# Kernel optimization log

Hardware: AMD Instinct MI355X
Metric: run time of the kernel (lower is better)

## Reference

```python
import jax, jax.numpy as jnp
import numpy as np

VEC = 64
HEADS = 16
DUP = 4
HIDDEN = VEC * HEADS * DUP  # 4096
EPS = 1e-12


def setup_inputs() -> dict:
    key = jax.random.key(0)
    ks = jax.random.split(key, 7)
    B, S, N = 4, 512, 512
    out_len = VEC * HEADS
    return {
        "embeddings": jax.random.normal(ks[0], (B, S, HIDDEN), jnp.float32),
        "keys": jax.random.normal(ks[1], (B, N, out_len), jnp.float32),
        "values": jax.random.normal(ks[2], (B, N, out_len), jnp.float32),
        "Wq": jax.random.normal(ks[3], (HIDDEN, HIDDEN), jnp.float32) * (1.0 / np.sqrt(HIDDEN)),
        "bq": jnp.zeros((HIDDEN,), jnp.float32),
        "Wre": jax.random.normal(ks[4], (HIDDEN, HIDDEN), jnp.float32) * (1.0 / np.sqrt(HIDDEN)),
        "bre": jnp.zeros((HIDDEN,), jnp.float32),
        "ln_g": jnp.ones((HIDDEN,), jnp.float32),
        "ln_b": jnp.zeros((HIDDEN,), jnp.float32),
    }


def reference(embeddings, keys, values, Wq, bq, Wre, bre, ln_g, ln_b):
    B, S, _ = embeddings.shape
    N = keys.shape[1]
    # query projection: (B,S,hidden) -> reshape to (B, S*DUP, VEC, HEADS) -> (B,H,S*DUP,VEC)
    q = embeddings @ Wq.T + bq
    q = q.reshape(B, S * DUP, VEC, HEADS).transpose(0, 3, 1, 2)
    # keys: (B,N,VEC*HEADS) -> (B,H,VEC,N); values -> (B,H,N,VEC)
    k = keys.reshape(B, N, VEC, HEADS).transpose(0, 3, 2, 1)
    v = values.reshape(B, N, VEC, HEADS).transpose(0, 3, 1, 2)
    scores = jnp.matmul(q, k) / np.sqrt(VEC).astype(np.float32)  # (B,H,S*DUP,N)
    probs = jax.nn.softmax(scores, axis=-1)
    out = jnp.matmul(probs, v)  # (B,H,S*DUP,VEC)
    # (B,H,S*DUP,VEC) -> (B,H,S,VEC*DUP) -> (B,S,H,VEC*DUP) -> (B,S,HIDDEN)
    out = out.reshape(B, HEADS, S, VEC * DUP).transpose(0, 2, 1, 3).reshape(B, S, HIDDEN)
    # LayerNorm (biased variance, torch semantics)
    mu = jnp.mean(out, axis=-1, keepdims=True)
    var = jnp.mean(jnp.square(out - mu), axis=-1, keepdims=True)
    ln = (out - mu) / jnp.sqrt(var + EPS) * ln_g + ln_b
    return ln @ Wre.T + bre
```

## Files before the change

### kernel.cpp

```cpp
#include <hip/hip_runtime.h>

typedef __attribute__((ext_vector_type(8))) _Float16 half8;
typedef __attribute__((ext_vector_type(4))) _Float16 half4;
typedef __attribute__((ext_vector_type(4))) float    floatx4;

#define GLD16(g, l)                                                            \
  __builtin_amdgcn_global_load_lds(                                            \
      (const __attribute__((address_space(1))) void*)(g),                      \
      (__attribute__((address_space(3))) void*)(l), 16, 0, 0)

__device__ __forceinline__ void cvt8(const float* __restrict__ in,
                                     _Float16* __restrict__ out, int i) {
  const float4* p = (const float4*)in + (size_t)i * 2;
  float4 a = p[0], b = p[1];
  half8 h;
  h[0] = (_Float16)a.x; h[1] = (_Float16)a.y; h[2] = (_Float16)a.z; h[3] = (_Float16)a.w;
  h[4] = (_Float16)b.x; h[5] = (_Float16)b.y; h[6] = (_Float16)b.z; h[7] = (_Float16)b.w;
  *(half8*)(out + (size_t)i * 8) = h;
}

__global__ __launch_bounds__(256) void prepA(const float* __restrict__ emb,
                                             const float* __restrict__ Wq,
                                             const float* __restrict__ keys,
                                             const float* __restrict__ values,
                                             _Float16* __restrict__ embH,
                                             _Float16* __restrict__ WqH,
                                             _Float16* __restrict__ Kh,
                                             _Float16* __restrict__ Vt) {
  const int bid = blockIdx.x, t = threadIdx.x;
  if (bid < 4096) {
    cvt8(emb, embH, bid * 256 + t);
  } else if (bid < 12288) {
    cvt8(Wq, WqH, (bid - 4096) * 256 + t);
  } else {
    const int tid = (bid - 12288) * 256 + t;
    {
      int v = tid & 63, n = (tid >> 6) & 511, h = (tid >> 15) & 15, b = tid >> 19;
      Kh[tid] = (_Float16)keys[((size_t)(b * 512 + n)) * 1024 + v * 16 + h];
    }
    {
      int n = tid & 511, v = (tid >> 9) & 63, h = (tid >> 15) & 15, b = tid >> 19;
      Vt[tid] = (_Float16)values[((size_t)(b * 512 + n)) * 1024 + v * 16 + h];
    }
  }
}

template <int MODE>
__global__ __launch_bounds__(256, 3) void gemm_bt(const _Float16* __restrict__ A,
                                                  const _Float16* __restrict__ Bw,
                                                  const float* __restrict__ bias,
                                                  float* __restrict__ Cf,
                                                  _Float16* __restrict__ H0,
                                                  _Float16* __restrict__ H1) {
  const int K = 4096;
  __shared__ _Float16 lA[128 * 64];
  __shared__ _Float16 lB[128 * 64];
  const int t = threadIdx.x, lane = t & 63, w = t >> 6;
  const int m0 = blockIdx.y * 128, n0 = blockIdx.x * 128;
  const int kb = blockIdx.z * 2048;
  const int wm = (w >> 1) * 64, wn = (w & 1) * 64;
  const int fr = lane & 15, fq = lane >> 4;

  floatx4 acc[4][4];
#pragma unroll
  for (int i = 0; i < 4; i++)
#pragma unroll
    for (int j = 0; j < 4; j++) acc[i][j] = (floatx4)(0.f);

  const int srow = t >> 3;
  const int sch = (t & 7) ^ (srow & 7);
  const _Float16* gA = A + (size_t)(m0 + srow) * K + kb + sch * 8;
  const _Float16* gB = Bw + (size_t)(n0 + srow) * K + kb + sch * 8;
  _Float16* dA = &lA[t * 8];
  _Float16* dB = &lB[t * 8];

  for (int k0 = 0; k0 < 2048; k0 += 64) {
    GLD16(gA, dA);
    GLD16(gA + (size_t)32 * K, dA + 2048);
    GLD16(gA + (size_t)64 * K, dA + 4096);
    GLD16(gA + (size_t)96 * K, dA + 6144);
    GLD16(gB, dB);
    GLD16(gB + (size_t)32 * K, dB + 2048);
    GLD16(gB + (size_t)64 * K, dB + 4096);
    GLD16(gB + (size_t)96 * K, dB + 6144);
    gA += 64;
    gB += 64;
    __syncthreads();
#pragma unroll
    for (int ks = 0; ks < 2; ks++) {
      half8 af[4], bf[4];
#pragma unroll
      for (int i = 0; i < 4; i++) {
        const int rr = wm + i * 16 + fr;
        af[i] = *(const half8*)&lA[rr * 64 + (((ks * 4 + fq) ^ (rr & 7)) * 8)];
      }
#pragma unroll
      for (int j = 0; j < 4; j++) {
        const int rr = wn + j * 16 + fr;
        bf[j] = *(const half8*)&lB[rr * 64 + (((ks * 4 + fq) ^ (rr & 7)) * 8)];
      }
#pragma unroll
      for (int i = 0; i < 4; i++)
#pragma unroll
        for (int j = 0; j < 4; j++)
          acc[i][j] =
              __builtin_amdgcn_mfma_f32_16x16x32_f16(af[i], bf[j], acc[i][j], 0, 0, 0);
    }
    __syncthreads();
  }

  const int z = blockIdx.z;
#pragma unroll
  for (int i = 0; i < 4; i++)
#pragma unroll
    for (int j = 0; j < 4; j++) {
      const int col = n0 + wn + j * 16 + fr;
      const int rbase = m0 + wm + i * 16 + fq * 4;
      if (MODE == 0 && z == 0) {
        const float bv = bias[col];
#pragma unroll
        for (int r = 0; r < 4; r++)
          Cf[(size_t)(rbase + r) * 4096 + col] = acc[i][j][r] + bv;
      } else {
        _Float16* P = z ? H1 : H0;
#pragma unroll
        for (int r = 0; r < 4; r++)
          P[(size_t)(rbase + r) * 4096 + col] = (_Float16)acc[i][j][r];
      }
    }
}

__global__ __launch_bounds__(256) void prepB(const float* __restrict__ Wre,
                                             _Float16* __restrict__ WreH,
                                             const _Float16* __restrict__ p0,
                                             const _Float16* __restrict__ p1,
                                             const float* __restrict__ bq,
                                             _Float16* __restrict__ q) {
  const int bid = blockIdx.x, t = threadIdx.x;
  if (bid < 8192) {
    cvt8(Wre, WreH, bid * 256 + t);
    return;
  }
  __shared__ _Float16 T[4][16][80];
  const int L = t & 63, w = t >> 6;
  const int m = bid - 8192, d = w;
  const int b = m >> 9, s = m & 511;
  const size_t src = (size_t)m * 4096 + d * 1024 + L * 16;
  half8 a0 = *(const half8*)(p0 + src);
  half8 a1 = *(const half8*)(p0 + src + 8);
  half8 b0 = *(const half8*)(p1 + src);
  half8 b1 = *(const half8*)(p1 + src + 8);
  const float4* bqv = (const float4*)(bq + d * 1024 + L * 16);
  float bias[16];
#pragma unroll
  for (int c = 0; c < 4; c++) {
    float4 f = bqv[c];
    bias[c * 4 + 0] = f.x; bias[c * 4 + 1] = f.y;
    bias[c * 4 + 2] = f.z; bias[c * 4 + 3] = f.w;
  }
#pragma unroll
  for (int h = 0; h < 8; h++) {
    T[w][h][L] = (_Float16)(((float)a0[h] + (float)b0[h] + bias[h]) * 0.125f);
    T[w][h + 8][L] =
        (_Float16)(((float)a1[h] + (float)b1[h] + bias[h + 8]) * 0.125f);
  }
  const int h2 = L >> 2, c2 = L & 3;
  _Float16* dst = q + (((size_t)(b * 16 + h2) * 2048) + s * 4 + d) * 64 + c2 * 8;
  *(half8*)dst = *(const half8*)&T[w][h2][c2 * 8];
  *(half8*)(dst + 32) = *(const half8*)&T[w][h2][32 + c2 * 8];
}

__global__ __launch_bounds__(256) void combine2(float* __restrict__ out,
                                                const _Float16* __restrict__ p1) {
  const int i4 = (blockIdx.x * 256 + threadIdx.x) * 4;
  float4 o = *(float4*)&out[i4];
  half4 p = *(const half4*)(p1 + i4);
  o.x += (float)p[0];
  o.y += (float)p[1];
  o.z += (float)p[2];
  o.w += (float)p[3];
  *(float4*)&out[i4] = o;
}

__global__ __launch_bounds__(256) void attn_mfma(const _Float16* __restrict__ Q,
                                                 const _Float16* __restrict__ Kh,
                                                 const _Float16* __restrict__ Vt,
                                                 float* __restrict__ Out) {
  __shared__ _Float16 Pbuf[4][32][136];
  const int t = threadIdx.x, lane = t & 63, w = t >> 6;
  const int fr = lane & 15, fq = lane >> 4;
  const int bh = blockIdx.y, qt = blockIdx.x;
  const int b = bh >> 4, h = bh & 15;

  const _Float16* Qb = Q + ((size_t)bh * 2048 + qt * 128 + w * 32) * 64;
  const _Float16* Kb = Kh + (size_t)bh * 512 * 64;
  const _Float16* Vb = Vt + (size_t)bh * 64 * 512;

  half8 qf[2][2];
#pragma unroll
  for (int i = 0; i < 2; i++)
#pragma unroll
    for (int ks = 0; ks < 2; ks++)
      qf[i][ks] = *(const half8*)(Qb + (i * 16 + fr) * 64 + ks * 32 + fq * 8);

  floatx4 oacc[2][4];
  float l_acc[2][4];
#pragma unroll
  for (int i = 0; i < 2; i++)
#pragma unroll
    for (int j = 0; j < 4; j++) {
      oacc[i][j] = (floatx4)(0.f);
      l_acc[i][j] = 0.f;
    }

  for (int c0 = 0; c0 < 512; c0 += 128) {
    floatx4 sc[2][8];
#pragma unroll
    for (int i = 0; i < 2; i++)
#pragma unroll
      for (int j = 0; j < 8; j++) sc[i][j] = (floatx4)(0.f);
#pragma unroll
    for (int j = 0; j < 8; j++) {
      const _Float16* kr = Kb + (size_t)(c0 + j * 16 + fr) * 64 + fq * 8;
      half8 k0 = *(const half8*)kr;
      half8 k1 = *(const half8*)(kr + 32);
#pragma unroll
      for (int i = 0; i < 2; i++) {
        sc[i][j] = __builtin_amdgcn_mfma_f32_16x16x32_f16(qf[i][0], k0, sc[i][j], 0, 0, 0);
        sc[i][j] = __builtin_amdgcn_mfma_f32_16x16x32_f16(qf[i][1], k1, sc[i][j], 0, 0, 0);
      }
    }
#pragma unroll
    for (int i = 0; i < 2; i++)
#pragma unroll
      for (int j = 0; j < 8; j++)
#pragma unroll
        for (int r = 0; r < 4; r++) {
          float p = __expf(sc[i][j][r]);
          l_acc[i][r] += p;
          Pbuf[w][i * 16 + fq * 4 + r][j * 16 + fr] = (_Float16)p;
        }
#pragma unroll
    for (int kn = 0; kn < 4; kn++) {
      half8 pa[2];
#pragma unroll
      for (int i = 0; i < 2; i++)
        pa[i] = *(const half8*)&Pbuf[w][i * 16 + fr][kn * 32 + fq * 8];
#pragma unroll
      for (int jv = 0; jv < 4; jv++) {
        half8 vb = *(const half8*)(Vb + (size_t)(jv * 16 + fr) * 512 + c0 + kn * 32 + fq * 8);
#pragma unroll
        for (int i = 0; i < 2; i++)
          oacc[i][jv] = __builtin_amdgcn_mfma_f32_16x16x32_f16(pa[i], vb, oacc[i][jv], 0, 0, 0);
      }
    }
  }

#pragma unroll
  for (int i = 0; i < 2; i++)
#pragma unroll
    for (int r = 0; r < 4; r++) {
#pragma unroll
      for (int m = 8; m; m >>= 1)
        l_acc[i][r] += __shfl_xor(l_acc[i][r], m, 16);
    }
#pragma unroll
  for (int i = 0; i < 2; i++) {
#pragma unroll
    for (int r = 0; r < 4; r++) {
      const float inv = 1.f / l_acc[i][r];
      const int m2 = qt * 128 + w * 32 + i * 16 + fq * 4 + r;
      float* orow = Out + ((size_t)(b * 512 + (m2 >> 2))) * 4096 + h * 256 + (m2 & 3) * 64 + fr;
#pragma unroll
      for (int jv = 0; jv < 4; jv++) orow[jv * 16] = oacc[i][jv][r] * inv;
    }
  }
}

__global__ __launch_bounds__(256) void ln_kernel(const float* __restrict__ X,
                                                 const float* __restrict__ g,
                                                 const float* __restrict__ bb,
                                                 _Float16* __restrict__ Y) {
  const int row = blockIdx.x;
  const int t = threadIdx.x;
  const float* x = X + (size_t)row * 4096;
  float4 vals[4];
  float sum = 0.f, sq = 0.f;
#pragma unroll
  for (int c = 0; c < 4; c++) {
    vals[c] = *(const float4*)&x[c * 1024 + t * 4];
    sum += vals[c].x + vals[c].y + vals[c].z + vals[c].w;
    sq += vals[c].x * vals[c].x + vals[c].y * vals[c].y + vals[c].z * vals[c].z +
          vals[c].w * vals[c].w;
  }
#pragma unroll
  for (int off = 32; off > 0; off >>= 1) {
    sum += __shfl_down(sum, off, 64);
    sq += __shfl_down(sq, off, 64);
  }
  __shared__ float red[8];
  const int w = t >> 6;
  if ((t & 63) == 0) {
    red[w] = sum;
    red[4 + w] = sq;
  }
  __syncthreads();
  sum = red[0] + red[1] + red[2] + red[3];
  sq = red[4] + red[5] + red[6] + red[7];
  const float mu = sum * (1.f / 4096.f);
  float var = sq * (1.f / 4096.f) - mu * mu;
  var = fmaxf(var, 0.f);
  const float rstd = rsqrtf(var + 1e-12f);
#pragma unroll
  for (int c = 0; c < 4; c++) {
    const int j = c * 1024 + t * 4;
    float4 gg = *(const float4*)&g[j];
    float4 bv = *(const float4*)&bb[j];
    half4 y;
    y[0] = (_Float16)((vals[c].x - mu) * rstd * gg.x + bv.x);
    y[1] = (_Float16)((vals[c].y - mu) * rstd * gg.y + bv.y);
    y[2] = (_Float16)((vals[c].z - mu) * rstd * gg.z + bv.z);
    y[3] = (_Float16)((vals[c].w - mu) * rstd * gg.w + bv.w);
    *(half4*)&Y[(size_t)row * 4096 + j] = y;
  }
}

extern "C" void kernel_launch(void* const* d_in, const int* in_sizes, int n_in,
                              void* d_out, int out_size, void* d_ws,
                              size_t ws_size, hipStream_t stream) {
  const float* emb = (const float*)d_in[0];
  const float* keys = (const float*)d_in[1];
  const float* values = (const float*)d_in[2];
  const float* Wq = (const float*)d_in[3];
  const float* bq = (const float*)d_in[4];
  const float* Wre = (const float*)d_in[5];
  const float* bre = (const float*)d_in[6];
  const float* ln_g = (const float*)d_in[7];
  const float* ln_b = (const float*)d_in[8];
  float* out = (float*)d_out;

  char* ws = (char*)d_ws;
  _Float16* embH = (_Float16*)(ws);
  _Float16* WqH = (_Float16*)(ws + ((size_t)16 << 20));
  _Float16* Kh = (_Float16*)(ws + ((size_t)48 << 20));
  _Float16* Vt = (_Float16*)(ws + ((size_t)52 << 20));
  _Float16* P0q = (_Float16*)d_out;
  _Float16* P1q = (_Float16*)((char*)d_out + ((size_t)16 << 20));
  _Float16* WreH = WqH;
  _Float16* qattn = (_Float16*)(ws);
  _Float16* lnH = (_Float16*)(ws + ((size_t)48 << 20));
  _Float16* P1o = (_Float16*)(ws);

  prepA<<<20480, 256, 0, stream>>>(emb, Wq, keys, values, embH, WqH, Kh, Vt);
  gemm_bt<1><<<dim3(32, 16, 2), 256, 0, stream>>>(embH, WqH, nullptr, nullptr,
                                                  P0q, P1q);
  prepB<<<10240, 256, 0, stream>>>(Wre, WreH, P0q, P1q, bq, qattn);
  attn_mfma<<<dim3(16, 64), 256, 0, stream>>>(qattn, Kh, Vt, out);
  ln_kernel<<<2048, 256, 0, stream>>>(out, ln_g, ln_b, lnH);
  gemm_bt<0><<<dim3(32, 16, 2), 256, 0, stream>>>(lnH, WreH, bre, out, nullptr,
                                                  P1o);
  combine2<<<8192, 256, 0, stream>>>(out, P1o);
}
```

Before: 482.6 us.

## Rewrite GEMM as 256x256 tile, 8-wave, double-buffered pipelined LDS kernel

The split-K GEMM grows from 128x128 tiles with 4 waves to 256x256 tiles with 8 waves, each wave holding an 8x4 MFMA accumulator block. Global-to-LDS loads are double-buffered and issued in interleaved quarter-stages between MFMA groups, with explicit vmcnt waits, barriers and setprio. The aim is to hide load latency behind the matrix core work and to reuse each staged tile more. In exchange it uses far more LDS and registers per block, and the grid shrinks to 256 blocks, which may underfill the CUs.

```diff
diff --git a/kernel.cpp b/kernel.cpp
--- a/kernel.cpp
+++ b/kernel.cpp
@@ -8,6 +8,8 @@
   __builtin_amdgcn_global_load_lds(                                            \
       (const __attribute__((address_space(1))) void*)(g),                      \
       (__attribute__((address_space(3))) void*)(l), 16, 0, 0)
+
+#define MFMA16(a, b, c) __builtin_amdgcn_mfma_f32_16x16x32_f16(a, b, c, 0, 0, 0)
 
 __device__ __forceinline__ void cvt8(const float* __restrict__ in,
                                      _Float16* __restrict__ out, int i) {
@@ -46,26 +48,21 @@
 }
 
 template <int MODE>
-__global__ __launch_bounds__(256, 3) void gemm_bt(const _Float16* __restrict__ A,
+__global__ __launch_bounds__(512, 2) void gemm_bt(const _Float16* __restrict__ A,
                                                   const _Float16* __restrict__ Bw,
                                                   const float* __restrict__ bias,
                                                   float* __restrict__ Cf,
                                                   _Float16* __restrict__ H0,
                                                   _Float16* __restrict__ H1) {
   const int K = 4096;
-  __shared__ _Float16 lA[128 * 64];
-  __shared__ _Float16 lB[128 * 64];
+  const int NT = 32;
+  __shared__ _Float16 lA[2 * 16384];
+  __shared__ _Float16 lB[2 * 16384];
   const int t = threadIdx.x, lane = t & 63, w = t >> 6;
-  const int m0 = blockIdx.y * 128, n0 = blockIdx.x * 128;
+  const int m0 = blockIdx.y * 256, n0 = blockIdx.x * 256;
   const int kb = blockIdx.z * 2048;
-  const int wm = (w >> 1) * 64, wn = (w & 1) * 64;
+  const int wm = (w >> 2) * 128, wn = (w & 3) * 64;
   const int fr = lane & 15, fq = lane >> 4;
-
-  floatx4 acc[4][4];
-#pragma unroll
-  for (int i = 0; i < 4; i++)
-#pragma unroll
-    for (int j = 0; j < 4; j++) acc[i][j] = (floatx4)(0.f);
 
   const int srow = t >> 3;
   const int sch = (t & 7) ^ (srow & 7);
@@ -74,44 +71,96 @@
   _Float16* dA = &lA[t * 8];
   _Float16* dB = &lB[t * 8];
 
-  for (int k0 = 0; k0 < 2048; k0 += 64) {
-    GLD16(gA, dA);
-    GLD16(gA + (size_t)32 * K, dA + 2048);
-    GLD16(gA + (size_t)64 * K, dA + 4096);
-    GLD16(gA + (size_t)96 * K, dA + 6144);
-    GLD16(gB, dB);
-    GLD16(gB + (size_t)32 * K, dB + 2048);
-    GLD16(gB + (size_t)64 * K, dB + 4096);
-    GLD16(gB + (size_t)96 * K, dB + 6144);
-    gA += 64;
-    gB += 64;
-    __syncthreads();
-#pragma unroll
-    for (int ks = 0; ks < 2; ks++) {
-      half8 af[4], bf[4];
-#pragma unroll
-      for (int i = 0; i < 4; i++) {
-        const int rr = wm + i * 16 + fr;
-        af[i] = *(const half8*)&lA[rr * 64 + (((ks * 4 + fq) ^ (rr & 7)) * 8)];
-      }
-#pragma unroll
-      for (int j = 0; j < 4; j++) {
-        const int rr = wn + j * 16 + fr;
-        bf[j] = *(const half8*)&lB[rr * 64 + (((ks * 4 + fq) ^ (rr & 7)) * 8)];
-      }
-#pragma unroll
-      for (int i = 0; i < 4; i++)
-#pragma unroll
-        for (int j = 0; j < 4; j++)
-          acc[i][j] =
-              __builtin_amdgcn_mfma_f32_16x16x32_f16(af[i], bf[j], acc[i][j], 0, 0, 0);
-    }
-    __syncthreads();
+#define STG(op, bf_, kt_, h_)                                                  \
+  do {                                                                         \
+    const _Float16* g_ = (op ? gB : gA) + (size_t)((h_)*128) * K + (kt_)*64;   \
+    _Float16* d_ = (op ? dB : dA) + (bf_)*16384 + (h_)*8192;                   \
+    GLD16(g_, d_);                                                             \
+    GLD16(g_ + (size_t)64 * K, d_ + 4096);                                     \
+  } while (0)
+
+  STG(0, 0, 0, 0); STG(0, 0, 0, 1); STG(1, 0, 0, 0); STG(1, 0, 0, 1);
+  asm volatile("s_waitcnt vmcnt(4)" ::: "memory");
+  STG(0, 1, 1, 0); STG(0, 1, 1, 1); STG(1, 1, 1, 0);
+
+  floatx4 acc[8][4];
+#pragma unroll
+  for (int i = 0; i < 8; i++)
+#pragma unroll
+    for (int j = 0; j < 4; j++) acc[i][j] = (floatx4)(0.f);
+
+  const _Float16* cA = lA + (wm + fr) * 64;
+  const _Float16* cB = lB + (wn + fr) * 64;
+  const int xo0 = ((fq) ^ (fr & 7)) * 8;
+  const int xo1 = ((4 + fq) ^ (fr & 7)) * 8;
+
+  asm volatile("s_waitcnt vmcnt(6)" ::: "memory");
+  __builtin_amdgcn_s_barrier();
+
+#define QUAD(ibase, jbase)                                                     \
+  do {                                                                         \
+    __builtin_amdgcn_s_setprio(1);                                             \
+    _Pragma("unroll") for (int i_ = 0; i_ < 4; i_++) {                         \
+      _Pragma("unroll") for (int jj_ = 0; jj_ < 2; jj_++) {                    \
+        acc[(ibase) + i_][(jbase) + jj_] =                                     \
+            MFMA16(af[(ibase) + i_][0], bf[jj_][0], acc[(ibase) + i_][(jbase) + jj_]); \
+        acc[(ibase) + i_][(jbase) + jj_] =                                     \
+            MFMA16(af[(ibase) + i_][1], bf[jj_][1], acc[(ibase) + i_][(jbase) + jj_]); \
+      }                                                                        \
+    }                                                                          \
+    __builtin_amdgcn_s_setprio(0);                                             \
+  } while (0)
+
+  for (int tt = 0; tt < NT; ++tt) {
+    const int buf = tt & 1;
+    const int o = buf * 16384;
+    const int kt1 = tt + 1 < NT ? tt + 1 : NT - 1;
+    const int kt2 = tt + 2 < NT ? tt + 2 : NT - 1;
+    half8 af[8][2], bf[2][2];
+
+#pragma unroll
+    for (int i = 0; i < 8; i++) {
+      af[i][0] = *(const half8*)(cA + o + i * 1024 + xo0);
+      af[i][1] = *(const half8*)(cA + o + i * 1024 + xo1);
+    }
+#pragma unroll
+    for (int jj = 0; jj < 2; jj++) {
+      bf[jj][0] = *(const half8*)(cB + o + jj * 1024 + xo0);
+      bf[jj][1] = *(const half8*)(cB + o + jj * 1024 + xo1);
+    }
+    STG(1, (tt + 1) & 1, kt1, 1);
+    __builtin_amdgcn_s_barrier();
+    asm volatile("s_waitcnt lgkmcnt(0)" ::: "memory");
+    __builtin_amdgcn_sched_barrier(0);
+    QUAD(0, 0);
+    __builtin_amdgcn_s_barrier();
+
+    STG(0, buf, kt2, 0);
+    __builtin_amdgcn_s_barrier();
+    QUAD(4, 0);
+    __builtin_amdgcn_s_barrier();
+
+    bf[0][0] = *(const half8*)(cB + o + 2 * 1024 + xo0);
+    bf[0][1] = *(const half8*)(cB + o + 2 * 1024 + xo1);
+    bf[1][0] = *(const half8*)(cB + o + 3 * 1024 + xo0);
+    bf[1][1] = *(const half8*)(cB + o + 3 * 1024 + xo1);
+    STG(0, buf, kt2, 1);
+    __builtin_amdgcn_s_barrier();
+    asm volatile("s_waitcnt lgkmcnt(0)" ::: "memory");
+    __builtin_amdgcn_sched_barrier(0);
+    QUAD(0, 2);
+    __builtin_amdgcn_s_barrier();
+
+    STG(1, buf, kt2, 0);
+    __builtin_amdgcn_s_barrier();
+    QUAD(4, 2);
+    asm volatile("s_waitcnt vmcnt(6)" ::: "memory");
+    __builtin_amdgcn_s_barrier();
   }
 
   const int z = blockIdx.z;
 #pragma unroll
-  for (int i = 0; i < 4; i++)
+  for (int i = 0; i < 8; i++)
 #pragma unroll
     for (int j = 0; j < 4; j++) {
       const int col = n0 + wn + j * 16 + fr;
@@ -128,6 +177,8 @@
           P[(size_t)(rbase + r) * 4096 + col] = (_Float16)acc[i][j][r];
       }
     }
+#undef QUAD
+#undef STG
 }
 
 __global__ __launch_bounds__(256) void prepB(const float* __restrict__ Wre,
@@ -352,12 +403,12 @@
   _Float16* P1o = (_Float16*)(ws);
 
   prepA<<<20480, 256, 0, stream>>>(emb, Wq, keys, values, embH, WqH, Kh, Vt);
-  gemm_bt<1><<<dim3(32, 16, 2), 256, 0, stream>>>(embH, WqH, nullptr, nullptr,
-                                                  P0q, P1q);
+  gemm_bt<1><<<dim3(16, 8, 2), 512, 0, stream>>>(embH, WqH, nullptr, nullptr,
+                                                 P0q, P1q);
   prepB<<<10240, 256, 0, stream>>>(Wre, WreH, P0q, P1q, bq, qattn);
   attn_mfma<<<dim3(16, 64), 256, 0, stream>>>(qattn, Kh, Vt, out);
   ln_kernel<<<2048, 256, 0, stream>>>(out, ln_g, ln_b, lnH);
-  gemm_bt<0><<<dim3(32, 16, 2), 256, 0, stream>>>(lnH, WreH, bre, out, nullptr,
-                                                  P1o);
+  gemm_bt<0><<<dim3(16, 8, 2), 512, 0, stream>>>(lnH, WreH, bre, out, nullptr,
+                                                 P1o);
   combine2<<<8192, 256, 0, stream>>>(out, P1o);
 }
```

Result: faster. 463.5 us (-4.0%).
